# Kernel tuning notes

Measured on AMD Instinct MI355X. Metric: run time of the kernel, lower is better.

The kernel has to match this reference:

```python
import jax, jax.numpy as jnp
import numpy as np

V = 1_000_000        # max_id + 1
DIM = 128
B_PAIRS = 131072
NUM_NEGS = 8
B_IN = 65536


def _make_table(key):
    # tf.truncated_normal_initializer(stddev=1/sqrt(dim))
    std = 1.0 / (DIM ** 0.5)
    return jax.random.truncated_normal(key, -2.0, 2.0, (V, DIM), dtype=jnp.float32) * std


def setup_inputs() -> dict:
    key = jax.random.key(0)
    k1, k2, k3, k4, k5, k6 = jax.random.split(key, 6)
    return {
        "inputs": jax.random.randint(k1, (B_IN,), 0, V, dtype=jnp.int32),
        "src": jax.random.randint(k2, (B_PAIRS, 1), 0, V, dtype=jnp.int32),
        "pos": jax.random.randint(k3, (B_PAIRS, 1), 0, V, dtype=jnp.int32),
        "negs": jax.random.randint(k4, (B_PAIRS, NUM_NEGS), 0, V, dtype=jnp.int32),
        "target_table": _make_table(k5),
        "context_table": _make_table(k6),
    }


def reference(inputs, src, pos, negs, target_table, context_table):
    emb = target_table[src]            # [B, 1, D]
    emb_pos = context_table[pos]       # [B, 1, D]
    emb_negs = context_table[negs]     # [B, N, D]

    # decoder: per-pair dot products (batched matmul with transpose_b)
    logits = jnp.einsum("bid,bjd->bij", emb, emb_pos)        # [B, 1, 1]
    neg_logits = jnp.einsum("bid,bnd->bin", emb, emb_negs)   # [B, 1, N]

    # sigmoid_cross_entropy_with_logits: labels=1 -> softplus(-x); labels=0 -> softplus(x)
    loss = jnp.sum(jax.nn.softplus(-logits)) + jnp.sum(jax.nn.softplus(neg_logits))

    # mrr_score: positive placed last; ties broken toward negatives (lower index)
    ranks = 1 + jnp.sum(neg_logits >= logits, axis=-1)        # [B, 1]
    mrr = jnp.mean(1.0 / ranks.astype(jnp.float32))

    embedding = target_table[inputs]           # [B_IN, D]
    context_embedding = context_table[inputs]  # [B_IN, D]
    return embedding, context_embedding, loss, mrr
```

## Files before the change

kernel.cpp:

```cpp
#include <hip/hip_runtime.h>
#include <math.h>


constexpr int DIM  = 128;
constexpr int NNEG = 8;

typedef float f32x4 __attribute__((ext_vector_type(4)));

__global__ __launch_bounds__(256) void fused(
    const int*   __restrict__ inputs,
    const int*   __restrict__ src,
    const int*   __restrict__ pos,
    const int*   __restrict__ negs,
    const float* __restrict__ tgt,
    const float* __restrict__ ctx,
    float*       __restrict__ out_emb,
    float*       __restrict__ out_ctx,
    float*       __restrict__ partials,
    int b_in,
    int n_pairs)
{
    const int tid     = blockIdx.x * blockDim.x + threadIdx.x;
    const int nthread = gridDim.x * blockDim.x;

    {
        const int total = b_in * 64;
        for (int u = tid; u < total; u += nthread) {
            int row   = u >> 6;
            int sub   = u & 63;
            int table = sub >> 5;
            int lane  = sub & 31;
            size_t idx = (size_t)inputs[row];
            const f32x4* s = (const f32x4*)((table ? ctx : tgt) + idx * DIM);
            f32x4 v = __builtin_nontemporal_load(s + lane);
            f32x4* d = (f32x4*)((table ? out_ctx : out_emb) + (size_t)row * DIM);
            __builtin_nontemporal_store(v, d + lane);
        }
    }

    const int l16 = threadIdx.x & 15;
    const int b   = tid >> 4;

    float loss = 0.0f, mrr = 0.0f;
    if (b < n_pairs) {
        int sidx = src[b];
        const float4* srow = (const float4*)(tgt + (size_t)sidx * DIM);
        float4 e0 = srow[l16 * 2 + 0];
        float4 e1 = srow[l16 * 2 + 1];

        int ci[1 + NNEG];
        ci[0] = pos[b];
        const int4* np = (const int4*)(negs + (size_t)b * NNEG);
        int4 n0 = np[0];
        int4 n1 = np[1];
        ci[1] = n0.x; ci[2] = n0.y; ci[3] = n0.z; ci[4] = n0.w;
        ci[5] = n1.x; ci[6] = n1.y; ci[7] = n1.z; ci[8] = n1.w;

        float p[1 + NNEG];
#pragma unroll
        for (int c = 0; c < 1 + NNEG; ++c) {
            const float4* crow = (const float4*)(ctx + (size_t)ci[c] * DIM);
            float4 c0 = crow[l16 * 2 + 0];
            float4 c1 = crow[l16 * 2 + 1];
            p[c] = e0.x * c0.x + e0.y * c0.y + e0.z * c0.z + e0.w * c0.w
                 + e1.x * c1.x + e1.y * c1.y + e1.z * c1.z + e1.w * c1.w;
        }

#pragma unroll
        for (int c = 0; c < 1 + NNEG; ++c) {
#pragma unroll
            for (int off = 8; off > 0; off >>= 1)
                p[c] += __shfl_xor(p[c], off, 16);
        }

        float lg   = p[0];
        float prod = 1.0f + __expf(-lg);
        int rank = 1;
#pragma unroll
        for (int n = 1; n <= NNEG; ++n) {
            prod *= 1.0f + __expf(p[n]);
            rank += (p[n] >= lg) ? 1 : 0;
        }
        loss = __logf(prod);
        mrr  = 1.0f / (float)rank;
    }

#pragma unroll
    for (int off = 32; off > 0; off >>= 1) {
        loss += __shfl_xor(loss, off);
        mrr  += __shfl_xor(mrr,  off);
    }
    __shared__ float red[2 * 4];
    const int wib = threadIdx.x >> 6;
    if ((threadIdx.x & 63) == 0) {
        red[wib * 2 + 0] = loss * 0.0625f;
        red[wib * 2 + 1] = mrr  * 0.0625f;
    }
    __syncthreads();
    if (threadIdx.x == 0) {
        float Ls = 0.0f, Ms = 0.0f;
#pragma unroll
        for (int w = 0; w < 4; ++w) { Ls += red[2 * w]; Ms += red[2 * w + 1]; }
        partials[blockIdx.x * 2 + 0] = Ls;
        partials[blockIdx.x * 2 + 1] = Ms;
    }
}

__global__ __launch_bounds__(256) void finalize(
    const float* __restrict__ partials,
    float*       __restrict__ scalars,
    int nblocks,
    float inv_n)
{
    float L = 0.0f, M = 0.0f;
    for (int i = threadIdx.x; i < nblocks; i += 256) {
        L += partials[2 * i + 0];
        M += partials[2 * i + 1];
    }
#pragma unroll
    for (int off = 32; off > 0; off >>= 1) {
        L += __shfl_xor(L, off);
        M += __shfl_xor(M, off);
    }
    __shared__ float red[2 * 4];
    const int wib = threadIdx.x >> 6;
    if ((threadIdx.x & 63) == 0) {
        red[wib * 2 + 0] = L;
        red[wib * 2 + 1] = M;
    }
    __syncthreads();
    if (threadIdx.x == 0) {
        float Ls = 0.0f, Ms = 0.0f;
#pragma unroll
        for (int w = 0; w < 4; ++w) { Ls += red[2 * w]; Ms += red[2 * w + 1]; }
        scalars[0] = Ls;
        scalars[1] = Ms * inv_n;
    }
}

extern "C" void kernel_launch(void* const* d_in, const int* in_sizes, int n_in,
                              void* d_out, int out_size, void* d_ws, size_t ws_size,
                              hipStream_t stream) {
    const int*   inputs = (const int*)d_in[0];
    const int*   src    = (const int*)d_in[1];
    const int*   pos    = (const int*)d_in[2];
    const int*   negs   = (const int*)d_in[3];
    const float* tgt    = (const float*)d_in[4];
    const float* ctx    = (const float*)d_in[5];

    const int b_in    = in_sizes[0];
    const int b_pairs = in_sizes[1];

    float* out      = (float*)d_out;
    float* out_emb  = out;
    float* out_ctx  = out + (size_t)b_in * DIM;
    float* scalars  = out + (size_t)2 * b_in * DIM;
    float* partials = (float*)d_ws;

    const int blocks = (b_pairs * 16 + 255) / 256;
    fused<<<blocks, 256, 0, stream>>>(inputs, src, pos, negs, tgt, ctx,
                                      out_emb, out_ctx, partials,
                                      b_in, b_pairs);
    finalize<<<1, 256, 0, stream>>>(partials, scalars, blocks,
                                    1.0f / (float)b_pairs);
}
```

Before: 134.1 us.

## Use grid-stride persistent loop over pairs with fixed grid and nontemporal index loads

```diff
diff --git a/kernel.cpp b/kernel.cpp
--- a/kernel.cpp
+++ b/kernel.cpp
@@ -6,8 +6,9 @@
 constexpr int NNEG = 8;
 
 typedef float f32x4 __attribute__((ext_vector_type(4)));
+typedef int   i32x4 __attribute__((ext_vector_type(4)));
 
-__global__ __launch_bounds__(256) void fused(
+__global__ __launch_bounds__(256, 8) void fused(
     const int*   __restrict__ inputs,
     const int*   __restrict__ src,
     const int*   __restrict__ pos,
@@ -38,30 +39,34 @@
         }
     }
 
-    const int l16 = threadIdx.x & 15;
-    const int b   = tid >> 4;
+    const int lane = threadIdx.x & 63;
+    const int l16  = threadIdx.x & 15;
+    const int gid  = tid >> 4;
+    const int ngroups = nthread >> 4;
 
-    float loss = 0.0f, mrr = 0.0f;
-    if (b < n_pairs) {
-        int sidx = src[b];
-        const float4* srow = (const float4*)(tgt + (size_t)sidx * DIM);
-        float4 e0 = srow[l16 * 2 + 0];
-        float4 e1 = srow[l16 * 2 + 1];
+    float loss_acc = 0.0f;
+    float mrr_acc  = 0.0f;
+
+    for (int b = gid; b < n_pairs; b += ngroups) {
+        int sidx = __builtin_nontemporal_load(src + b);
+        const f32x4* srow = (const f32x4*)(tgt + (size_t)sidx * DIM);
+        f32x4 e0 = __builtin_nontemporal_load(srow + l16 * 2 + 0);
+        f32x4 e1 = __builtin_nontemporal_load(srow + l16 * 2 + 1);
 
         int ci[1 + NNEG];
-        ci[0] = pos[b];
-        const int4* np = (const int4*)(negs + (size_t)b * NNEG);
-        int4 n0 = np[0];
-        int4 n1 = np[1];
+        ci[0] = __builtin_nontemporal_load(pos + b);
+        const i32x4* np = (const i32x4*)(negs + (size_t)b * NNEG);
+        i32x4 n0 = __builtin_nontemporal_load(np + 0);
+        i32x4 n1 = __builtin_nontemporal_load(np + 1);
         ci[1] = n0.x; ci[2] = n0.y; ci[3] = n0.z; ci[4] = n0.w;
         ci[5] = n1.x; ci[6] = n1.y; ci[7] = n1.z; ci[8] = n1.w;
 
         float p[1 + NNEG];
 #pragma unroll
         for (int c = 0; c < 1 + NNEG; ++c) {
-            const float4* crow = (const float4*)(ctx + (size_t)ci[c] * DIM);
-            float4 c0 = crow[l16 * 2 + 0];
-            float4 c1 = crow[l16 * 2 + 1];
+            const f32x4* crow = (const f32x4*)(ctx + (size_t)ci[c] * DIM);
+            f32x4 c0 = crow[l16 * 2 + 0];
+            f32x4 c1 = crow[l16 * 2 + 1];
             p[c] = e0.x * c0.x + e0.y * c0.y + e0.z * c0.z + e0.w * c0.w
                  + e1.x * c1.x + e1.y * c1.y + e1.z * c1.z + e1.w * c1.w;
         }
@@ -81,20 +86,22 @@
             prod *= 1.0f + __expf(p[n]);
             rank += (p[n] >= lg) ? 1 : 0;
         }
-        loss = __logf(prod);
-        mrr  = 1.0f / (float)rank;
+        loss_acc += __logf(prod);
+        mrr_acc  += 1.0f / (float)rank;
     }
 
+    loss_acc *= 0.0625f;
+    mrr_acc  *= 0.0625f;
 #pragma unroll
     for (int off = 32; off > 0; off >>= 1) {
-        loss += __shfl_xor(loss, off);
-        mrr  += __shfl_xor(mrr,  off);
+        loss_acc += __shfl_xor(loss_acc, off);
+        mrr_acc  += __shfl_xor(mrr_acc,  off);
     }
     __shared__ float red[2 * 4];
     const int wib = threadIdx.x >> 6;
-    if ((threadIdx.x & 63) == 0) {
-        red[wib * 2 + 0] = loss * 0.0625f;
-        red[wib * 2 + 1] = mrr  * 0.0625f;
+    if (lane == 0) {
+        red[wib * 2 + 0] = loss_acc;
+        red[wib * 2 + 1] = mrr_acc;
     }
     __syncthreads();
     if (threadIdx.x == 0) {
@@ -157,7 +164,7 @@
     float* scalars  = out + (size_t)2 * b_in * DIM;
     float* partials = (float*)d_ws;
 
-    const int blocks = (b_pairs * 16 + 255) / 256;
+    const int blocks = 2048;
     fused<<<blocks, 256, 0, stream>>>(inputs, src, pos, negs, tgt, ctx,
                                       out_emb, out_ctx, partials,
                                       b_in, b_pairs);
```

New measurement: 249.3 us. 85.9% more time.
